# Performance work log

Measured on AMD Instinct MI355X. Metric: run time of the kernel, lower is better.

## Reference

```python
import jax, jax.numpy as jnp
import numpy as np

N = 50000      # nodes
E = 800000     # edges (avg degree 16)
D = 128        # node_embedding_dim
H = 256        # hidden_dim


def setup_inputs() -> dict:
    key = jax.random.key(0)
    ks = jax.random.split(key, 12)
    init = lambda k, shape, fan: (jax.random.normal(k, shape, jnp.float32) / np.sqrt(fan).astype(np.float32))
    return {
        "node_ids": jnp.arange(N, dtype=jnp.int32),
        "edge_index": jax.random.randint(ks[0], (2, E), 0, N, jnp.int32),
        "neighbour_edge_index": jax.random.randint(ks[1], (2, E), 0, N, jnp.int32),
        "edge_attr": jax.random.uniform(ks[2], (E,), jnp.float32),
        "emb": init(ks[3], (N, D), D),          # Embedding table
        "W_in": init(ks[4], (D, H), D), "b_in": jnp.zeros((H,), jnp.float32),
        "W_out": init(ks[5], (H, D), H), "b_out": jnp.zeros((D,), jnp.float32),
        "W1": init(ks[6], (2 * D, D), 2 * D), "b1": jnp.zeros((D,), jnp.float32),
        "W2": init(ks[7], (D, D), D), "b2": jnp.zeros((D,), jnp.float32),
        "W3": init(ks[8], (D, 1), D), "b3": jnp.zeros((1,), jnp.float32),
    }


def gcn_conv(x, W, b, edge_index, w):
    """PyG GCNConv, add_self_loops=False, normalize=True.
    out_i = b + sum_{(j->i)} d_i^{-1/2} w_ji d_j^{-1/2} (x_j @ W)
    deg_i = sum of incoming edge weights at target node i.
    """
    row, col = edge_index[0], edge_index[1]
    deg = jax.ops.segment_sum(w, col, num_segments=N)
    dinv = jnp.where(deg > 0, 1.0 / jnp.sqrt(deg), 0.0)
    norm = dinv[row] * w * dinv[col]                    # [E]
    h = x @ W                                           # [N, out]
    msg = h[row] * norm[:, None]                        # [E, out]
    return jax.ops.segment_sum(msg, col, num_segments=N) + b


def reference(node_ids, edge_index, neighbour_edge_index, edge_attr,
              emb, W_in, b_in, W_out, b_out, W1, b1, W2, b2, W3, b3):
    x = emb[node_ids]                                   # embedding lookup [N, D]
    x = jax.nn.elu(gcn_conv(x, W_in, b_in, edge_index, edge_attr))
    ones = jnp.ones((neighbour_edge_index.shape[1],), x.dtype)
    x = jax.nn.elu(gcn_conv(x, W_out, b_out, neighbour_edge_index, ones))
    # edge-level gather-concat-MLP decoder
    src, dst = edge_index[0], edge_index[1]
    h = jnp.concatenate([x[src], x[dst]], axis=1)       # [E, 2D]
    h = jax.nn.relu(h @ W1 + b1)
    h = jax.nn.relu(h @ W2 + b2)
    return (h @ W3 + b3).squeeze(-1)                    # [E]
```

## Files before the change

### kernel.cpp

```cpp
#include <hip/hip_runtime.h>
#include <math.h>

#define NN 50000
#define NE 800000

typedef __attribute__((ext_vector_type(8))) short s8_t;
typedef __attribute__((ext_vector_type(4))) float f4_t;

__device__ __forceinline__ short bf16_rne(float v) {
  unsigned u = __float_as_uint(v);
  unsigned r = (u + 0x7FFFu + ((u >> 16) & 1u)) >> 16;
  return (short)r;
}
__device__ __forceinline__ float bf16_tof(short h) {
  return __uint_as_float(((unsigned)(unsigned short)h) << 16);
}
__device__ __forceinline__ void split2(float v, short& hi, short& lo) {
  hi = bf16_rne(v);
  lo = bf16_rne(v - bf16_tof(hi));
}


__global__ __launch_bounds__(256) void k_wcvt(const float* __restrict__ W1,
                                              const float* __restrict__ W2,
                                              short* __restrict__ w1th,
                                              short* __restrict__ w1tl,
                                              short* __restrict__ w2th,
                                              short* __restrict__ w2tl) {
  int i = blockIdx.x * 256 + threadIdx.x;
  if (i < 32768) {
    int k = i >> 7, n = i & 127;
    short h, l; split2(W1[i], h, l);
    w1th[n * 256 + k] = h; w1tl[n * 256 + k] = l;
  } else if (i < 49152) {
    int j = i - 32768;
    int k = j >> 7, n = j & 127;
    short h, l; split2(W2[j], h, l);
    w2th[n * 128 + k] = h; w2tl[n * 128 + k] = l;
  }
}


__global__ __launch_bounds__(256) void k_hist(const int* __restrict__ ei,
                                              const int* __restrict__ nei,
                                              const float* __restrict__ w,
                                              int* __restrict__ cnt1,
                                              float* __restrict__ deg1,
                                              int* __restrict__ cnt2) {
  int e = blockIdx.x * 256 + threadIdx.x;
  if (e < NE) {
    int c1 = ei[NE + e];
    atomicAdd(&cnt1[c1], 1);
    atomicAdd(&deg1[c1], w[e]);
    atomicAdd(&cnt2[nei[NE + e]], 1);
  }
}

__global__ __launch_bounds__(256) void k_dinvs(const float* __restrict__ deg1,
                                               const int* __restrict__ cnt2,
                                               float* __restrict__ dinv1,
                                               float* __restrict__ dinv2) {
  int i = blockIdx.x * 256 + threadIdx.x;
  if (i < NN) {
    float d1 = deg1[i];
    dinv1[i] = d1 > 0.f ? (1.0f / sqrtf(d1)) : 0.f;
    int c2 = cnt2[i];
    dinv2[i] = c2 > 0 ? (1.0f / sqrtf((float)c2)) : 0.f;
  }
}


#define NCHUNK 196

__global__ __launch_bounds__(256) void k_scan_part(const int* __restrict__ cnt1,
                                                   const int* __restrict__ cnt2,
                                                   int* __restrict__ part) {
  int g = blockIdx.x >= NCHUNK;
  int chunk = g ? blockIdx.x - NCHUNK : blockIdx.x;
  const int* cnt = g ? cnt2 : cnt1;
  int i = chunk * 256 + threadIdx.x;
  int v = (i < NN) ? cnt[i] : 0;
  __shared__ int sd[4];
#pragma unroll
  for (int o = 32; o; o >>= 1) v += __shfl_down(v, o);
  if ((threadIdx.x & 63) == 0) sd[threadIdx.x >> 6] = v;
  __syncthreads();
  if (threadIdx.x == 0) part[blockIdx.x] = sd[0] + sd[1] + sd[2] + sd[3];
}

__global__ __launch_bounds__(256) void k_scan_mid(int* __restrict__ part,
                                                  int* __restrict__ off1_last,
                                                  int* __restrict__ off2_last) {
  __shared__ int sd[256];
  for (int g = 0; g < 2; g++) {
    int base = g * NCHUNK;
    int v = (threadIdx.x < NCHUNK) ? part[base + threadIdx.x] : 0;
    sd[threadIdx.x] = v;
    __syncthreads();
    for (int o = 1; o < 256; o <<= 1) {
      int x = (threadIdx.x >= o) ? sd[threadIdx.x - o] : 0;
      __syncthreads();
      sd[threadIdx.x] += x;
      __syncthreads();
    }
    if (threadIdx.x < NCHUNK) part[base + threadIdx.x] = sd[threadIdx.x] - v;
    if (threadIdx.x == 255) *(g ? off2_last : off1_last) = sd[255];
    __syncthreads();
  }
}

__global__ __launch_bounds__(256) void k_scan_final(const int* __restrict__ cnt1,
                                                    const int* __restrict__ cnt2,
                                                    const int* __restrict__ part,
                                                    int* __restrict__ off1,
                                                    int* __restrict__ pos1,
                                                    int* __restrict__ off2,
                                                    int* __restrict__ pos2) {
  int g = blockIdx.x >= NCHUNK;
  int chunk = g ? blockIdx.x - NCHUNK : blockIdx.x;
  const int* cnt = g ? cnt2 : cnt1;
  int* off = g ? off2 : off1;
  int* pos = g ? pos2 : pos1;
  __shared__ int sd[256];
  int i = chunk * 256 + threadIdx.x;
  int v = (i < NN) ? cnt[i] : 0;
  sd[threadIdx.x] = v;
  __syncthreads();
  for (int o = 1; o < 256; o <<= 1) {
    int x = (threadIdx.x >= o) ? sd[threadIdx.x - o] : 0;
    __syncthreads();
    sd[threadIdx.x] += x;
    __syncthreads();
  }
  if (i < NN) {
    int ex = part[blockIdx.x] + sd[threadIdx.x] - v;
    off[i] = ex; pos[i] = ex;
  }
}


__global__ __launch_bounds__(256) void k_fill(const int* __restrict__ ei,
                                              const int* __restrict__ nei,
                                              const float* __restrict__ w,
                                              const float* __restrict__ dinv1,
                                              const float* __restrict__ dinv2,
                                              int* __restrict__ pos1,
                                              int* __restrict__ csr1_src,
                                              float* __restrict__ csr1_nrm,
                                              int* __restrict__ pos2,
                                              int* __restrict__ csr2_src,
                                              float* __restrict__ csr2_nrm) {
  int e = blockIdx.x * 256 + threadIdx.x;
  if (e < NE) {
    int r = ei[e], c = ei[NE + e];
    float nv = dinv1[r] * w[e] * dinv1[c];
    int s = atomicAdd(&pos1[c], 1);
    csr1_src[s] = r; csr1_nrm[s] = nv;
    int r2 = nei[e], c2 = nei[NE + e];
    float nv2 = dinv2[r2] * dinv2[c2];
    int s2 = atomicAdd(&pos2[c2], 1);
    csr2_src[s2] = r2; csr2_nrm[s2] = nv2;
  }
}


__global__ __launch_bounds__(256) void k_agg1(const int* __restrict__ off,
                                              const int* __restrict__ csr_src,
                                              const float* __restrict__ csr_nrm,
                                              const int* __restrict__ ids,
                                              const float* __restrict__ emb,
                                              float* __restrict__ aggX) {
  int wave = threadIdx.x >> 6, lane = threadIdx.x & 63;
  int node = blockIdx.x * 4 + wave;
  int start = off[node], end = off[node + 1];
  float2 acc = make_float2(0.f, 0.f);
  int i = start;
  for (; i + 1 < end; i += 2) {
    int s0 = csr_src[i], s1 = csr_src[i + 1];
    float n0 = csr_nrm[i], n1 = csr_nrm[i + 1];
    float2 v0 = *(const float2*)(emb + (size_t)ids[s0] * 128 + lane * 2);
    float2 v1 = *(const float2*)(emb + (size_t)ids[s1] * 128 + lane * 2);
    acc.x = fmaf(n0, v0.x, fmaf(n1, v1.x, acc.x));
    acc.y = fmaf(n0, v0.y, fmaf(n1, v1.y, acc.y));
  }
  if (i < end) {
    int s0 = csr_src[i];
    float n0 = csr_nrm[i];
    float2 v0 = *(const float2*)(emb + (size_t)ids[s0] * 128 + lane * 2);
    acc.x = fmaf(n0, v0.x, acc.x);
    acc.y = fmaf(n0, v0.y, acc.y);
  }
  *(float2*)(aggX + (size_t)node * 128 + lane * 2) = acc;
}


__global__ __launch_bounds__(256) void k_agg2(const int* __restrict__ off,
                                              const int* __restrict__ csr_src,
                                              const float* __restrict__ csr_nrm,
                                              const float* __restrict__ h2,
                                              const float* __restrict__ b,
                                              short* __restrict__ xh,
                                              short* __restrict__ xl) {
  int wave = threadIdx.x >> 6, lane = threadIdx.x & 63;
  int node = blockIdx.x * 4 + wave;
  int start = off[node], end = off[node + 1];
  float2 acc = make_float2(0.f, 0.f);
  int i = start;
  for (; i + 1 < end; i += 2) {
    int s0 = csr_src[i], s1 = csr_src[i + 1];
    float n0 = csr_nrm[i], n1 = csr_nrm[i + 1];
    float2 v0 = *(const float2*)(h2 + (size_t)s0 * 128 + lane * 2);
    float2 v1 = *(const float2*)(h2 + (size_t)s1 * 128 + lane * 2);
    acc.x = fmaf(n0, v0.x, fmaf(n1, v1.x, acc.x));
    acc.y = fmaf(n0, v0.y, fmaf(n1, v1.y, acc.y));
  }
  if (i < end) {
    int s0 = csr_src[i];
    float n0 = csr_nrm[i];
    float2 v0 = *(const float2*)(h2 + (size_t)s0 * 128 + lane * 2);
    acc.x = fmaf(n0, v0.x, acc.x);
    acc.y = fmaf(n0, v0.y, acc.y);
  }
  float vx = acc.x + b[lane * 2];
  float vy = acc.y + b[lane * 2 + 1];
  vx = vx > 0.f ? vx : expm1f(vx);
  vy = vy > 0.f ? vy : expm1f(vy);
  short hx, lx, hy, ly;
  split2(vx, hx, lx);
  split2(vy, hy, ly);
  unsigned hp = (unsigned)(unsigned short)hx | ((unsigned)(unsigned short)hy << 16);
  unsigned lp = (unsigned)(unsigned short)lx | ((unsigned)(unsigned short)ly << 16);
  *(unsigned*)(xh + (size_t)node * 128 + lane * 2) = hp;
  *(unsigned*)(xl + (size_t)node * 128 + lane * 2) = lp;
}


__global__ __launch_bounds__(256) void k_gemm_aggin(const float* __restrict__ X,
                                                    const float* __restrict__ W,
                                                    const float* __restrict__ b,
                                                    float* __restrict__ C) {
  __shared__ float As[32][128];
  int r0 = blockIdx.x * 32;
  int t = threadIdx.x;
  for (int i = t; i < 1024; i += 256) {
    int r = i >> 5, q = (i & 31) << 2;
    int rr = r0 + r;
    float4 v = make_float4(0.f, 0.f, 0.f, 0.f);
    if (rr < NN) v = *(const float4*)(X + (size_t)rr * 128 + q);
    *(float4*)(&As[r][q]) = v;
  }
  __syncthreads();
  int tc = t & 31, tr = t >> 5;
  int c0 = tc * 8, rr0 = tr * 4;
  float acc[4][8];
#pragma unroll
  for (int r = 0; r < 4; r++)
#pragma unroll
    for (int c = 0; c < 8; c++) acc[r][c] = 0.f;

  for (int k0 = 0; k0 < 128; k0 += 4) {
    float a_[4][4];
#pragma unroll
    for (int r = 0; r < 4; r++) {
      float4 v = *(const float4*)(&As[rr0 + r][k0]);
      a_[r][0] = v.x; a_[r][1] = v.y; a_[r][2] = v.z; a_[r][3] = v.w;
    }
#pragma unroll
    for (int kk = 0; kk < 4; kk++) {
      float4 w0 = *(const float4*)(W + (size_t)(k0 + kk) * 256 + c0);
      float4 w1 = *(const float4*)(W + (size_t)(k0 + kk) * 256 + c0 + 4);
#pragma unroll
      for (int r = 0; r < 4; r++) {
        float av = a_[r][kk];
        acc[r][0] += av * w0.x; acc[r][1] += av * w0.y;
        acc[r][2] += av * w0.z; acc[r][3] += av * w0.w;
        acc[r][4] += av * w1.x; acc[r][5] += av * w1.y;
        acc[r][6] += av * w1.z; acc[r][7] += av * w1.w;
      }
    }
  }
  float4 bb0 = *(const float4*)(b + c0);
  float4 bb1 = *(const float4*)(b + c0 + 4);
#pragma unroll
  for (int r = 0; r < 4; r++) {
    int rr = r0 + rr0 + r;
    if (rr < NN) {
      float o[8];
      o[0] = acc[r][0] + bb0.x; o[1] = acc[r][1] + bb0.y;
      o[2] = acc[r][2] + bb0.z; o[3] = acc[r][3] + bb0.w;
      o[4] = acc[r][4] + bb1.x; o[5] = acc[r][5] + bb1.y;
      o[6] = acc[r][6] + bb1.z; o[7] = acc[r][7] + bb1.w;
#pragma unroll
      for (int c = 0; c < 8; c++) o[c] = o[c] > 0.f ? o[c] : expm1f(o[c]);
      *(float4*)(C + (size_t)rr * 256 + c0) = make_float4(o[0], o[1], o[2], o[3]);
      *(float4*)(C + (size_t)rr * 256 + c0 + 4) = make_float4(o[4], o[5], o[6], o[7]);
    }
  }
}


__global__ __launch_bounds__(256) void k_gemm_mid(const float* __restrict__ X,
                                                  const float* __restrict__ W,
                                                  float* __restrict__ C) {
  __shared__ float As[32][256];
  int r0 = blockIdx.x * 32;
  int t = threadIdx.x;
  for (int i = t; i < 2048; i += 256) {
    int r = i >> 6, q = (i & 63) << 2;
    int rr = r0 + r;
    float4 v = make_float4(0.f, 0.f, 0.f, 0.f);
    if (rr < NN) v = *(const float4*)(X + (size_t)rr * 256 + q);
    *(float4*)(&As[r][q]) = v;
  }
  __syncthreads();
  int tc = t & 31, tr = t >> 5;
  int c0 = tc * 4, rr0 = tr * 4;
  float acc[4][4];
#pragma unroll
  for (int r = 0; r < 4; r++)
#pragma unroll
    for (int c = 0; c < 4; c++) acc[r][c] = 0.f;

  for (int k0 = 0; k0 < 256; k0 += 4) {
    float a_[4][4];
#pragma unroll
    for (int r = 0; r < 4; r++) {
      float4 v = *(const float4*)(&As[rr0 + r][k0]);
      a_[r][0] = v.x; a_[r][1] = v.y; a_[r][2] = v.z; a_[r][3] = v.w;
    }
#pragma unroll
    for (int kk = 0; kk < 4; kk++) {
      float4 w = *(const float4*)(W + (size_t)(k0 + kk) * 128 + c0);
#pragma unroll
      for (int r = 0; r < 4; r++) {
        float av = a_[r][kk];
        acc[r][0] += av * w.x; acc[r][1] += av * w.y;
        acc[r][2] += av * w.z; acc[r][3] += av * w.w;
      }
    }
  }
#pragma unroll
  for (int r = 0; r < 4; r++) {
    int rr = r0 + rr0 + r;
    if (rr < NN) {
      float4 o = make_float4(acc[r][0], acc[r][1], acc[r][2], acc[r][3]);
      *(float4*)(C + (size_t)rr * 128 + c0) = o;
    }
  }
}


__global__ __launch_bounds__(256) void k_pab(const short* __restrict__ x2h,
                                             const short* __restrict__ x2l,
                                             const short* __restrict__ w1th,
                                             const short* __restrict__ w1tl,
                                             float* __restrict__ Pa,
                                             float* __restrict__ Pb) {
  __shared__ short Xh[32 * 136];
  __shared__ short Xl[32 * 136];
  int t = threadIdx.x;
  int n0 = blockIdx.x * 32;
#pragma unroll
  for (int j = 0; j < 2; j++) {
    int i = t + 256 * j;
    int row = i >> 4, q = i & 15;
    int node = n0 + row; if (node >= NN) node = NN - 1;
    *(uint4*)&Xh[row * 136 + q * 8] = *(const uint4*)(x2h + (size_t)node * 128 + q * 8);
    *(uint4*)&Xl[row * 136 + q * 8] = *(const uint4*)(x2l + (size_t)node * 128 + q * 8);
  }
  __syncthreads();

  int w = t >> 6, lane = t & 63;
  int quad = lane >> 4, l16 = lane & 15;
  int nb = w * 32;
  int aoff0 = l16 * 136 + quad * 8;
  int aoff1 = (16 + l16) * 136 + quad * 8;
  int bo0 = (nb + l16) * 256 + quad * 8;
  int bo1 = (nb + 16 + l16) * 256 + quad * 8;

  f4_t aa[2][2], ab[2][2];
#pragma unroll
  for (int mi = 0; mi < 2; mi++)
#pragma unroll
    for (int ni = 0; ni < 2; ni++) {
      aa[mi][ni] = (f4_t){0.f, 0.f, 0.f, 0.f};
      ab[mi][ni] = (f4_t){0.f, 0.f, 0.f, 0.f};
    }

#pragma unroll
  for (int kb = 0; kb < 4; kb++) {
    int k0 = kb * 32;
    s8_t ah0 = *(const s8_t*)&Xh[aoff0 + k0];
    s8_t ah1 = *(const s8_t*)&Xh[aoff1 + k0];
    s8_t al0 = *(const s8_t*)&Xl[aoff0 + k0];
    s8_t al1 = *(const s8_t*)&Xl[aoff1 + k0];
    {
      s8_t bh0 = *(const s8_t*)(w1th + bo0 + k0);
      s8_t bh1 = *(const s8_t*)(w1th + bo1 + k0);
      s8_t bl0 = *(const s8_t*)(w1tl + bo0 + k0);
      s8_t bl1 = *(const s8_t*)(w1tl + bo1 + k0);
      aa[0][0] = __builtin_amdgcn_mfma_f32_16x16x32_bf16(ah0, bh0, aa[0][0], 0, 0, 0);
      aa[0][0] = __builtin_amdgcn_mfma_f32_16x16x32_bf16(ah0, bl0, aa[0][0], 0, 0, 0);
      aa[0][0] = __builtin_amdgcn_mfma_f32_16x16x32_bf16(al0, bh0, aa[0][0], 0, 0, 0);
      aa[0][1] = __builtin_amdgcn_mfma_f32_16x16x32_bf16(ah0, bh1, aa[0][1], 0, 0, 0);
      aa[0][1] = __builtin_amdgcn_mfma_f32_16x16x32_bf16(ah0, bl1, aa[0][1], 0, 0, 0);
      aa[0][1] = __builtin_amdgcn_mfma_f32_16x16x32_bf16(al0, bh1, aa[0][1], 0, 0, 0);
      aa[1][0] = __builtin_amdgcn_mfma_f32_16x16x32_bf16(ah1, bh0, aa[1][0], 0, 0, 0);
      aa[1][0] = __builtin_amdgcn_mfma_f32_16x16x32_bf16(ah1, bl0, aa[1][0], 0, 0, 0);
      aa[1][0] = __builtin_amdgcn_mfma_f32_16x16x32_bf16(al1, bh0, aa[1][0], 0, 0, 0);
      aa[1][1] = __builtin_amdgcn_mfma_f32_16x16x32_bf16(ah1, bh1, aa[1][1], 0, 0, 0);
      aa[1][1] = __builtin_amdgcn_mfma_f32_16x16x32_bf16(ah1, bl1, aa[1][1], 0, 0, 0);
      aa[1][1] = __builtin_amdgcn_mfma_f32_16x16x32_bf16(al1, bh1, aa[1][1], 0, 0, 0);
    }
    {
      s8_t bh0 = *(const s8_t*)(w1th + bo0 + 128 + k0);
      s8_t bh1 = *(const s8_t*)(w1th + bo1 + 128 + k0);
      s8_t bl0 = *(const s8_t*)(w1tl + bo0 + 128 + k0);
      s8_t bl1 = *(const s8_t*)(w1tl + bo1 + 128 + k0);
      ab[0][0] = __builtin_amdgcn_mfma_f32_16x16x32_bf16(ah0, bh0, ab[0][0], 0, 0, 0);
      ab[0][0] = __builtin_amdgcn_mfma_f32_16x16x32_bf16(ah0, bl0, ab[0][0], 0, 0, 0);
      ab[0][0] = __builtin_amdgcn_mfma_f32_16x16x32_bf16(al0, bh0, ab[0][0], 0, 0, 0);
      ab[0][1] = __builtin_amdgcn_mfma_f32_16x16x32_bf16(ah0, bh1, ab[0][1], 0, 0, 0);
      ab[0][1] = __builtin_amdgcn_mfma_f32_16x16x32_bf16(ah0, bl1, ab[0][1], 0, 0, 0);
      ab[0][1] = __builtin_amdgcn_mfma_f32_16x16x32_bf16(al0, bh1, ab[0][1], 0, 0, 0);
      ab[1][0] = __builtin_amdgcn_mfma_f32_16x16x32_bf16(ah1, bh0, ab[1][0], 0, 0, 0);
      ab[1][0] = __builtin_amdgcn_mfma_f32_16x16x32_bf16(ah1, bl0, ab[1][0], 0, 0, 0);
      ab[1][0] = __builtin_amdgcn_mfma_f32_16x16x32_bf16(al1, bh0, ab[1][0], 0, 0, 0);
      ab[1][1] = __builtin_amdgcn_mfma_f32_16x16x32_bf16(ah1, bh1, ab[1][1], 0, 0, 0);
      ab[1][1] = __builtin_amdgcn_mfma_f32_16x16x32_bf16(ah1, bl1, ab[1][1], 0, 0, 0);
      ab[1][1] = __builtin_amdgcn_mfma_f32_16x16x32_bf16(al1, bh1, ab[1][1], 0, 0, 0);
    }
  }

#pragma unroll
  for (int mi = 0; mi < 2; mi++)
#pragma unroll
    for (int ni = 0; ni < 2; ni++) {
      int col = nb + ni * 16 + l16;
#pragma unroll
      for (int r = 0; r < 4; r++) {
        int node = n0 + mi * 16 + quad * 4 + r;
        if (node < NN) {
          Pa[(size_t)node * 128 + col] = aa[mi][ni][r];
          Pb[(size_t)node * 128 + col] = ab[mi][ni][r];
        }
      }
    }
}


#define ST 136
#define S2 132

__global__ __launch_bounds__(256, 4) void k_decoder(
    const float* __restrict__ Pa, const float* __restrict__ Pb,
    const int* __restrict__ ei, const float* __restrict__ b1,
    const short* __restrict__ w2th, const short* __restrict__ w2tl,
    const float* __restrict__ b2,
    const float* __restrict__ W3, const float* __restrict__ b3,
    float* __restrict__ out) {
  __shared__ short ThTl[2 * 32 * ST];
  short* Th = ThTl;
  short* Tl = ThTl + 32 * ST;
  float* T2 = (float*)ThTl;

  int t = threadIdx.x;
  int e0 = blockIdx.x * 32;

#pragma unroll
  for (int j = 0; j < 2; j++) {
    int i = t + 256 * j;
    int le = i >> 4, q = i & 15;
    int src = ei[e0 + le], dst = ei[NE + e0 + le];
    const float* pa = Pa + (size_t)src * 128 + q * 8;
    const float* pb = Pb + (size_t)dst * 128 + q * 8;
    float4 a0 = *(const float4*)(pa);
    float4 a1 = *(const float4*)(pa + 4);
    float4 c0 = *(const float4*)(pb);
    float4 c1 = *(const float4*)(pb + 4);
    float4 d0 = *(const float4*)(b1 + q * 8);
    float4 d1 = *(const float4*)(b1 + q * 8 + 4);
    float v[8];
    v[0] = a0.x + c0.x + d0.x; v[1] = a0.y + c0.y + d0.y;
    v[2] = a0.z + c0.z + d0.z; v[3] = a0.w + c0.w + d0.w;
    v[4] = a1.x + c1.x + d1.x; v[5] = a1.y + c1.y + d1.y;
    v[6] = a1.z + c1.z + d1.z; v[7] = a1.w + c1.w + d1.w;
    s8_t hv, lv;
#pragma unroll
    for (int k = 0; k < 8; k++) {
      float x = fmaxf(v[k], 0.f);
      short h, l; split2(x, h, l);
      hv[k] = h; lv[k] = l;
    }
    *(s8_t*)&Th[le * ST + q * 8] = hv;
    *(s8_t*)&Tl[le * ST + q * 8] = lv;
  }
  __syncthreads();

  int w = t >> 6, lane = t & 63;
  int quad = lane >> 4, l16 = lane & 15;
  int nb = w * 32;
  float b2v0 = b2[nb + l16], b2v1 = b2[nb + 16 + l16];
  float b3v = b3[0];

  int toff0 = l16 * ST + quad * 8;
  int toff1 = (16 + l16) * ST + quad * 8;
  int coff0 = (nb + l16) * 128 + quad * 8;
  int coff1 = (nb + 16 + l16) * 128 + quad * 8;

  f4_t acc2[2][2];
#pragma unroll
  for (int mi = 0; mi < 2; mi++)
#pragma unroll
    for (int ni = 0; ni < 2; ni++) acc2[mi][ni] = (f4_t){0.f, 0.f, 0.f, 0.f};

#pragma unroll
  for (int kb = 0; kb < 4; kb++) {
    int k0 = kb * 32;
    s8_t ah0 = *(const s8_t*)&Th[toff0 + k0];
    s8_t ah1 = *(const s8_t*)&Th[toff1 + k0];
    s8_t al0 = *(const s8_t*)&Tl[toff0 + k0];
    s8_t al1 = *(const s8_t*)&Tl[toff1 + k0];
    s8_t bh0 = *(const s8_t*)(w2th + coff0 + k0);
    s8_t bh1 = *(const s8_t*)(w2th + coff1 + k0);
    s8_t bl0 = *(const s8_t*)(w2tl + coff0 + k0);
    s8_t bl1 = *(const s8_t*)(w2tl + coff1 + k0);
    acc2[0][0] = __builtin_amdgcn_mfma_f32_16x16x32_bf16(ah0, bh0, acc2[0][0], 0, 0, 0);
    acc2[0][0] = __builtin_amdgcn_mfma_f32_16x16x32_bf16(ah0, bl0, acc2[0][0], 0, 0, 0);
    acc2[0][0] = __builtin_amdgcn_mfma_f32_16x16x32_bf16(al0, bh0, acc2[0][0], 0, 0, 0);
    acc2[0][1] = __builtin_amdgcn_mfma_f32_16x16x32_bf16(ah0, bh1, acc2[0][1], 0, 0, 0);
    acc2[0][1] = __builtin_amdgcn_mfma_f32_16x16x32_bf16(ah0, bl1, acc2[0][1], 0, 0, 0);
    acc2[0][1] = __builtin_amdgcn_mfma_f32_16x16x32_bf16(al0, bh1, acc2[0][1], 0, 0, 0);
    acc2[1][0] = __builtin_amdgcn_mfma_f32_16x16x32_bf16(ah1, bh0, acc2[1][0], 0, 0, 0);
    acc2[1][0] = __builtin_amdgcn_mfma_f32_16x16x32_bf16(ah1, bl0, acc2[1][0], 0, 0, 0);
    acc2[1][0] = __builtin_amdgcn_mfma_f32_16x16x32_bf16(al1, bh0, acc2[1][0], 0, 0, 0);
    acc2[1][1] = __builtin_amdgcn_mfma_f32_16x16x32_bf16(ah1, bh1, acc2[1][1], 0, 0, 0);
    acc2[1][1] = __builtin_amdgcn_mfma_f32_16x16x32_bf16(ah1, bl1, acc2[1][1], 0, 0, 0);
    acc2[1][1] = __builtin_amdgcn_mfma_f32_16x16x32_bf16(al1, bh1, acc2[1][1], 0, 0, 0);
  }
  __syncthreads();

#pragma unroll
  for (int mi = 0; mi < 2; mi++)
#pragma unroll
    for (int ni = 0; ni < 2; ni++) {
      float bv = ni ? b2v1 : b2v0;
      int col = nb + ni * 16 + l16;
#pragma unroll
      for (int r = 0; r < 4; r++) {
        int row = mi * 16 + quad * 4 + r;
        T2[row * S2 + col] = fmaxf(acc2[mi][ni][r] + bv, 0.f);
      }
    }
  __syncthreads();

  {
    int le = t >> 3, j0 = (t & 7) * 16;
    float s = 0.f;
#pragma unroll
    for (int j = 0; j < 16; j += 4) {
      float4 v = *(const float4*)(&T2[le * S2 + j0 + j]);
      float4 wv = *(const float4*)(W3 + j0 + j);
      s += v.x * wv.x + v.y * wv.y + v.z * wv.z + v.w * wv.w;
    }
    s += __shfl_down(s, 4);
    s += __shfl_down(s, 2);
    s += __shfl_down(s, 1);
    if ((t & 7) == 0) out[e0 + le] = s + b3v;
  }
}


extern "C" void kernel_launch(void* const* d_in, const int* in_sizes, int n_in,
                              void* d_out, int out_size, void* d_ws, size_t ws_size,
                              hipStream_t stream) {
  const int*   node_ids = (const int*)d_in[0];
  const int*   ei       = (const int*)d_in[1];
  const int*   nei      = (const int*)d_in[2];
  const float* eattr    = (const float*)d_in[3];
  const float* emb      = (const float*)d_in[4];
  const float* W_in     = (const float*)d_in[5];
  const float* b_in     = (const float*)d_in[6];
  const float* W_out    = (const float*)d_in[7];
  const float* b_out    = (const float*)d_in[8];
  const float* W1       = (const float*)d_in[9];
  const float* b1       = (const float*)d_in[10];
  const float* W2       = (const float*)d_in[11];
  const float* b2       = (const float*)d_in[12];
  const float* W3       = (const float*)d_in[13];
  const float* b3       = (const float*)d_in[14];
  float* out = (float*)d_out;

  float* ws    = (float*)d_ws;
  float* bufA  = ws;
  float* bufB  = bufA + (size_t)NN * 128;
  int*   cnt1  = (int*)(bufB + (size_t)NN * 256);
  int*   cnt2  = cnt1 + NN;
  float* deg1  = (float*)(cnt2 + NN);
  float* dinv1 = deg1 + NN;
  float* dinv2 = dinv1 + NN;
  int*   off1  = (int*)(dinv2 + NN);
  int*   pos1  = off1 + NN + 1;
  int*   off2  = pos1 + NN;
  int*   pos2  = off2 + NN + 1;
  int*   c1src = pos2 + NN;
  float* c1nrm = (float*)(c1src + NE);
  int*   c2src = (int*)(c1nrm + NE);
  float* c2nrm = (float*)(c2src + NE);
  short* w1th  = (short*)(c2nrm + NE);
  short* w1tl  = w1th + 32768;
  short* w2th  = w1tl + 32768;
  short* w2tl  = w2th + 16384;
  int*   part  = (int*)(w2tl + 16384);

  float* aggX  = bufA;
  float* h2    = bufA;
  float* Pa    = bufA;
  float* x1    = bufB;
  short* x2h   = (short*)bufB;
  short* x2l   = x2h + (size_t)NN * 128;
  float* Pb    = bufB + (size_t)NN * 128;

  k_wcvt<<<192, 256, 0, stream>>>(W1, W2, w1th, w1tl, w2th, w2tl);

  hipMemsetAsync(cnt1, 0, 3 * (size_t)NN * sizeof(int), stream);
  k_hist<<<NE / 256, 256, 0, stream>>>(ei, nei, eattr, cnt1, deg1, cnt2);
  k_dinvs<<<(NN + 255) / 256, 256, 0, stream>>>(deg1, cnt2, dinv1, dinv2);
  k_scan_part<<<2 * NCHUNK, 256, 0, stream>>>(cnt1, cnt2, part);
  k_scan_mid<<<1, 256, 0, stream>>>(part, off1 + NN, off2 + NN);
  k_scan_final<<<2 * NCHUNK, 256, 0, stream>>>(cnt1, cnt2, part,
                                               off1, pos1, off2, pos2);
  k_fill<<<NE / 256, 256, 0, stream>>>(ei, nei, eattr, dinv1, dinv2,
                                       pos1, c1src, c1nrm, pos2, c2src, c2nrm);

  k_agg1<<<NN / 4, 256, 0, stream>>>(off1, c1src, c1nrm, node_ids, emb, aggX);
  k_gemm_aggin<<<(NN + 31) / 32, 256, 0, stream>>>(aggX, W_in, b_in, x1);

  k_gemm_mid<<<(NN + 31) / 32, 256, 0, stream>>>(x1, W_out, h2);
  k_agg2<<<NN / 4, 256, 0, stream>>>(off2, c2src, c2nrm, h2, b_out, x2h, x2l);

  k_pab<<<(NN + 31) / 32, 256, 0, stream>>>(x2h, x2l, w1th, w1tl, Pa, Pb);

  k_decoder<<<NE / 32, 256, 0, stream>>>(Pa, Pb, ei, b1,
                                         w2th, w2tl, b2, W3, b3, out);
}
```

Before: 864.7 us.

## Process decoder edges in destination-sorted CSR order and fold b1 into Pb

The decoder now walks edges in CSR order grouped by destination, using new csr dst and edge-id arrays written by k_fill, and scatters each output to its original edge index. Consecutive edges then share destination rows of Pb, which should improve cache reuse on that gather. The b1 bias is added once per node in k_pab instead of once per edge. The aggregation loops are also unrolled by four to keep more gathers in flight. In exchange, k_fill writes two extra arrays and the output stores become scattered.

```diff
diff --git a/kernel.cpp b/kernel.cpp
--- a/kernel.cpp
+++ b/kernel.cpp
@@ -147,6 +147,8 @@
                                               int* __restrict__ pos1,
                                               int* __restrict__ csr1_src,
                                               float* __restrict__ csr1_nrm,
+                                              int* __restrict__ csr1_dst,
+                                              int* __restrict__ csr1_eid,
                                               int* __restrict__ pos2,
                                               int* __restrict__ csr2_src,
                                               float* __restrict__ csr2_nrm) {
@@ -155,7 +157,7 @@
     int r = ei[e], c = ei[NE + e];
     float nv = dinv1[r] * w[e] * dinv1[c];
     int s = atomicAdd(&pos1[c], 1);
-    csr1_src[s] = r; csr1_nrm[s] = nv;
+    csr1_src[s] = r; csr1_nrm[s] = nv; csr1_dst[s] = c; csr1_eid[s] = e;
     int r2 = nei[e], c2 = nei[NE + e];
     float nv2 = dinv2[r2] * dinv2[c2];
     int s2 = atomicAdd(&pos2[c2], 1);
@@ -175,15 +177,17 @@
   int start = off[node], end = off[node + 1];
   float2 acc = make_float2(0.f, 0.f);
   int i = start;
-  for (; i + 1 < end; i += 2) {
-    int s0 = csr_src[i], s1 = csr_src[i + 1];
-    float n0 = csr_nrm[i], n1 = csr_nrm[i + 1];
+  for (; i + 3 < end; i += 4) {
+    int s0 = csr_src[i], s1 = csr_src[i + 1], s2 = csr_src[i + 2], s3 = csr_src[i + 3];
+    float n0 = csr_nrm[i], n1 = csr_nrm[i + 1], n2 = csr_nrm[i + 2], n3 = csr_nrm[i + 3];
     float2 v0 = *(const float2*)(emb + (size_t)ids[s0] * 128 + lane * 2);
     float2 v1 = *(const float2*)(emb + (size_t)ids[s1] * 128 + lane * 2);
-    acc.x = fmaf(n0, v0.x, fmaf(n1, v1.x, acc.x));
-    acc.y = fmaf(n0, v0.y, fmaf(n1, v1.y, acc.y));
-  }
-  if (i < end) {
+    float2 v2 = *(const float2*)(emb + (size_t)ids[s2] * 128 + lane * 2);
+    float2 v3 = *(const float2*)(emb + (size_t)ids[s3] * 128 + lane * 2);
+    acc.x = fmaf(n0, v0.x, fmaf(n1, v1.x, fmaf(n2, v2.x, fmaf(n3, v3.x, acc.x))));
+    acc.y = fmaf(n0, v0.y, fmaf(n1, v1.y, fmaf(n2, v2.y, fmaf(n3, v3.y, acc.y))));
+  }
+  for (; i < end; i++) {
     int s0 = csr_src[i];
     float n0 = csr_nrm[i];
     float2 v0 = *(const float2*)(emb + (size_t)ids[s0] * 128 + lane * 2);
@@ -206,15 +210,17 @@
   int start = off[node], end = off[node + 1];
   float2 acc = make_float2(0.f, 0.f);
   int i = start;
-  for (; i + 1 < end; i += 2) {
-    int s0 = csr_src[i], s1 = csr_src[i + 1];
-    float n0 = csr_nrm[i], n1 = csr_nrm[i + 1];
+  for (; i + 3 < end; i += 4) {
+    int s0 = csr_src[i], s1 = csr_src[i + 1], s2 = csr_src[i + 2], s3 = csr_src[i + 3];
+    float n0 = csr_nrm[i], n1 = csr_nrm[i + 1], n2 = csr_nrm[i + 2], n3 = csr_nrm[i + 3];
     float2 v0 = *(const float2*)(h2 + (size_t)s0 * 128 + lane * 2);
     float2 v1 = *(const float2*)(h2 + (size_t)s1 * 128 + lane * 2);
-    acc.x = fmaf(n0, v0.x, fmaf(n1, v1.x, acc.x));
-    acc.y = fmaf(n0, v0.y, fmaf(n1, v1.y, acc.y));
-  }
-  if (i < end) {
+    float2 v2 = *(const float2*)(h2 + (size_t)s2 * 128 + lane * 2);
+    float2 v3 = *(const float2*)(h2 + (size_t)s3 * 128 + lane * 2);
+    acc.x = fmaf(n0, v0.x, fmaf(n1, v1.x, fmaf(n2, v2.x, fmaf(n3, v3.x, acc.x))));
+    acc.y = fmaf(n0, v0.y, fmaf(n1, v1.y, fmaf(n2, v2.y, fmaf(n3, v3.y, acc.y))));
+  }
+  for (; i < end; i++) {
     int s0 = csr_src[i];
     float n0 = csr_nrm[i];
     float2 v0 = *(const float2*)(h2 + (size_t)s0 * 128 + lane * 2);
@@ -354,6 +360,7 @@
                                              const short* __restrict__ x2l,
                                              const short* __restrict__ w1th,
                                              const short* __restrict__ w1tl,
+                                             const float* __restrict__ b1,
                                              float* __restrict__ Pa,
                                              float* __restrict__ Pb) {
   __shared__ short Xh[32 * 136];
@@ -432,17 +439,19 @@
     }
   }
 
+  float b1v0 = b1[nb + l16], b1v1 = b1[nb + 16 + l16];
 #pragma unroll
   for (int mi = 0; mi < 2; mi++)
 #pragma unroll
     for (int ni = 0; ni < 2; ni++) {
       int col = nb + ni * 16 + l16;
+      float bv = ni ? b1v1 : b1v0;
 #pragma unroll
       for (int r = 0; r < 4; r++) {
         int node = n0 + mi * 16 + quad * 4 + r;
         if (node < NN) {
           Pa[(size_t)node * 128 + col] = aa[mi][ni][r];
-          Pb[(size_t)node * 128 + col] = ab[mi][ni][r];
+          Pb[(size_t)node * 128 + col] = ab[mi][ni][r] + bv;
         }
       }
     }
@@ -454,7 +463,8 @@
 
 __global__ __launch_bounds__(256, 4) void k_decoder(
     const float* __restrict__ Pa, const float* __restrict__ Pb,
-    const int* __restrict__ ei, const float* __restrict__ b1,
+    const int* __restrict__ c1src, const int* __restrict__ c1dst,
+    const int* __restrict__ c1eid,
     const short* __restrict__ w2th, const short* __restrict__ w2tl,
     const float* __restrict__ b2,
     const float* __restrict__ W3, const float* __restrict__ b3,
@@ -465,26 +475,24 @@
   float* T2 = (float*)ThTl;
 
   int t = threadIdx.x;
-  int e0 = blockIdx.x * 32;
+  int s0base = blockIdx.x * 32;
 
 #pragma unroll
   for (int j = 0; j < 2; j++) {
     int i = t + 256 * j;
     int le = i >> 4, q = i & 15;
-    int src = ei[e0 + le], dst = ei[NE + e0 + le];
+    int src = c1src[s0base + le], dst = c1dst[s0base + le];
     const float* pa = Pa + (size_t)src * 128 + q * 8;
     const float* pb = Pb + (size_t)dst * 128 + q * 8;
     float4 a0 = *(const float4*)(pa);
     float4 a1 = *(const float4*)(pa + 4);
     float4 c0 = *(const float4*)(pb);
     float4 c1 = *(const float4*)(pb + 4);
-    float4 d0 = *(const float4*)(b1 + q * 8);
-    float4 d1 = *(const float4*)(b1 + q * 8 + 4);
     float v[8];
-    v[0] = a0.x + c0.x + d0.x; v[1] = a0.y + c0.y + d0.y;
-    v[2] = a0.z + c0.z + d0.z; v[3] = a0.w + c0.w + d0.w;
-    v[4] = a1.x + c1.x + d1.x; v[5] = a1.y + c1.y + d1.y;
-    v[6] = a1.z + c1.z + d1.z; v[7] = a1.w + c1.w + d1.w;
+    v[0] = a0.x + c0.x; v[1] = a0.y + c0.y;
+    v[2] = a0.z + c0.z; v[3] = a0.w + c0.w;
+    v[4] = a1.x + c1.x; v[5] = a1.y + c1.y;
+    v[6] = a1.z + c1.z; v[7] = a1.w + c1.w;
     s8_t hv, lv;
 #pragma unroll
     for (int k = 0; k < 8; k++) {
@@ -566,7 +574,7 @@
     s += __shfl_down(s, 4);
     s += __shfl_down(s, 2);
     s += __shfl_down(s, 1);
-    if ((t & 7) == 0) out[e0 + le] = s + b3v;
+    if ((t & 7) == 0) out[c1eid[s0base + le]] = s + b3v;
   }
 }
 
@@ -605,7 +613,9 @@
   int*   pos2  = off2 + NN + 1;
   int*   c1src = pos2 + NN;
   float* c1nrm = (float*)(c1src + NE);
-  int*   c2src = (int*)(c1nrm + NE);
+  int*   c1dst = (int*)(c1nrm + NE);
+  int*   c1eid = c1dst + NE;
+  int*   c2src = c1eid + NE;
   float* c2nrm = (float*)(c2src + NE);
   short* w1th  = (short*)(c2nrm + NE);
   short* w1tl  = w1th + 32768;
@@ -631,7 +641,8 @@
   k_scan_final<<<2 * NCHUNK, 256, 0, stream>>>(cnt1, cnt2, part,
                                                off1, pos1, off2, pos2);
   k_fill<<<NE / 256, 256, 0, stream>>>(ei, nei, eattr, dinv1, dinv2,
-                                       pos1, c1src, c1nrm, pos2, c2src, c2nrm);
+                                       pos1, c1src, c1nrm, c1dst, c1eid,
+                                       pos2, c2src, c2nrm);
 
   k_agg1<<<NN / 4, 256, 0, stream>>>(off1, c1src, c1nrm, node_ids, emb, aggX);
   k_gemm_aggin<<<(NN + 31) / 32, 256, 0, stream>>>(aggX, W_in, b_in, x1);
@@ -639,8 +650,8 @@
   k_gemm_mid<<<(NN + 31) / 32, 256, 0, stream>>>(x1, W_out, h2);
   k_agg2<<<NN / 4, 256, 0, stream>>>(off2, c2src, c2nrm, h2, b_out, x2h, x2l);
 
-  k_pab<<<(NN + 31) / 32, 256, 0, stream>>>(x2h, x2l, w1th, w1tl, Pa, Pb);
-
-  k_decoder<<<NE / 32, 256, 0, stream>>>(Pa, Pb, ei, b1,
+  k_pab<<<(NN + 31) / 32, 256, 0, stream>>>(x2h, x2l, w1th, w1tl, b1, Pa, Pb);
+
+  k_decoder<<<NE / 32, 256, 0, stream>>>(Pa, Pb, c1src, c1dst, c1eid,
                                          w2th, w2tl, b2, W3, b3, out);
 }
```

Result: faster. 829.1 us (-4.1%).
